# Kernel tuning notes

Measured on AMD Instinct MI355X. Metric: run time of the kernel, lower is better.

Reference implementation:

```python
import jax, jax.numpy as jnp
import numpy as np
import math

N_FFT = 1024
HOP = 256
WIN = 1024
SR = 16000
N_MELS = 80
F_MIN = 0.0
F_MAX = 8000.0
N_STFT = N_FFT // 2 + 1


def _hz_to_mel_slaney(f):
    f = np.asarray(f, dtype=np.float64)
    logstep = math.log(6.4) / 27.0
    mel = 3.0 * f / 200.0
    return np.where(f >= 1000.0, 15.0 + np.log(np.maximum(f, 1e-10) / 1000.0) / logstep, mel)


def _mel_to_hz_slaney(m):
    m = np.asarray(m, dtype=np.float64)
    logstep = math.log(6.4) / 27.0
    f = 200.0 * m / 3.0
    return np.where(m >= 15.0, 1000.0 * np.exp(logstep * (m - 15.0)), f)


def _melscale_fbanks():
    # matches torchaudio.functional.melscale_fbanks(norm='slaney', mel_scale='slaney')
    all_freqs = np.linspace(0.0, SR / 2.0, N_STFT)
    m_min = _hz_to_mel_slaney(F_MIN)
    m_max = _hz_to_mel_slaney(F_MAX)
    m_pts = np.linspace(m_min, m_max, N_MELS + 2)
    f_pts = _mel_to_hz_slaney(m_pts)
    f_diff = f_pts[1:] - f_pts[:-1]                      # [n_mels+1]
    slopes = f_pts[None, :] - all_freqs[:, None]          # [n_freqs, n_mels+2]
    down = -slopes[:, :-2] / f_diff[:-1]
    up = slopes[:, 2:] / f_diff[1:]
    fb = np.maximum(0.0, np.minimum(down, up))            # [n_freqs, n_mels]
    enorm = 2.0 / (f_pts[2:N_MELS + 2] - f_pts[:N_MELS])  # slaney area normalization
    fb = fb * enorm[None, :]
    return fb.astype(np.float32)


def setup_inputs() -> dict:
    key = jax.random.key(0)
    wav = jax.random.normal(key, (32, 1, 160000), dtype=jnp.float32)
    # periodic Hann window
    n = np.arange(WIN)
    window = (0.5 * (1.0 - np.cos(2.0 * np.pi * n / WIN))).astype(np.float32)
    # real DFT matrices: angle = -2*pi*k*n/n_fft, k in [0, n_fft//2]
    k = np.arange(N_STFT, dtype=np.float64)
    nr = np.arange(N_FFT, dtype=np.float64)
    angle = -2.0 * np.pi * k[:, None] * nr[None, :] / N_FFT
    rfft_real = np.cos(angle).astype(np.float32)  # [N_STFT, N_FFT]
    rfft_imag = np.sin(angle).astype(np.float32)
    mel_fbanks = _melscale_fbanks()                # [N_STFT, N_MELS]
    return {
        "wav_with_channel": wav,
        "window": jnp.asarray(window),
        "mel_fbanks": jnp.asarray(mel_fbanks),
        "rfft_real": jnp.asarray(rfft_real),
        "rfft_imag": jnp.asarray(rfft_imag),
    }


def reference(wav_with_channel, window, mel_fbanks, rfft_real, rfft_imag):
    wav = wav_with_channel[:, 0, :]                      # [B, T]
    pad = N_FFT // 2
    padded = jnp.pad(wav, ((0, 0), (pad, pad)), mode="reflect")
    num_frames = (padded.shape[1] - WIN) // HOP + 1
    idx = jnp.arange(num_frames)[:, None] * HOP + jnp.arange(WIN)[None, :]  # [F, W]
    frames = padded[:, idx]                              # [B, F, W]
    windowed = frames * window                           # broadcast [W]
    # matmul-based real DFT (win_length == n_fft, power == 1.0)
    real = jnp.einsum("bfw,kw->bfk", windowed, rfft_real)
    imag = jnp.einsum("bfw,kw->bfk", windowed, rfft_imag)
    magnitude = jnp.sqrt(real * real + imag * imag)      # [B, F, N_STFT]
    mel = jnp.einsum("bfk,km->bfm", magnitude, mel_fbanks)  # [B, F, N_MELS]
    return jnp.transpose(mel, (0, 2, 1))                 # [B, N_MELS, F]
```

## Files before the change

kernel.cpp:

```cpp
#include <hip/hip_runtime.h>

#define WAVLEN   160000
#define NFRAMES  626
#define NFFT     1024
#define HOP      256
#define NSTFT    513
#define NMELS    80
#define FBLKS    157
#define PAD(i)   ((i) + ((i) >> 3))
#define BUFSZ    576
#define PWSTRIDE 49
#define PWTOT    (NMELS * PWSTRIDE)

__device__ __forceinline__ float2 cadd(float2 a, float2 b){ return make_float2(a.x+b.x, a.y+b.y); }
__device__ __forceinline__ float2 csub(float2 a, float2 b){ return make_float2(a.x-b.x, a.y-b.y); }
__device__ __forceinline__ float2 cmul(float2 a, float2 b){
    return make_float2(fmaf(a.x, b.x, -a.y*b.y), fmaf(a.x, b.y, a.y*b.x));
}
__device__ __forceinline__ float2 mulnegi(float2 a){ return make_float2(a.y, -a.x); }

__device__ __forceinline__ void fft4(float2& a0, float2& a1, float2& a2, float2& a3) {
    float2 t0 = cadd(a0, a2), t1 = csub(a0, a2);
    float2 t2 = cadd(a1, a3), t3 = csub(a1, a3);
    a0 = cadd(t0, t2); a2 = csub(t0, t2);
    float2 nt3 = mulnegi(t3);
    a1 = cadd(t1, nt3); a3 = csub(t1, nt3);
}

__device__ __forceinline__ void fft8(float2 v[8]) {
    float2 e0=v[0], e1=v[2], e2=v[4], e3=v[6];
    float2 o0=v[1], o1=v[3], o2=v[5], o3=v[7];
    fft4(e0,e1,e2,e3);
    fft4(o0,o1,o2,o3);
    const float C = 0.70710678118654752f;
    float2 w1o = make_float2(C*(o1.x + o1.y), C*(o1.y - o1.x));
    float2 w2o = mulnegi(o2);
    float2 w3o = make_float2(C*(o3.y - o3.x), -C*(o3.x + o3.y));
    v[0] = cadd(e0, o0);  v[4] = csub(e0, o0);
    v[1] = cadd(e1, w1o); v[5] = csub(e1, w1o);
    v[2] = cadd(e2, w2o); v[6] = csub(e2, w2o);
    v[3] = cadd(e3, w3o); v[7] = csub(e3, w3o);
}

__device__ __forceinline__ int2 mel_range(int m) {
    const float LOGSTEP = 0.06875177742094912f;
    const float MSTEP   = 0.55858524f;
    float mlo = (float)m * MSTEP;
    float mhi = (float)(m + 2) * MSTEP;
    float flo = (mlo < 15.f) ? 66.6666667f * mlo : 1000.f * expf(LOGSTEP * (mlo - 15.f));
    float fhi = (mhi < 15.f) ? 66.6666667f * mhi : 1000.f * expf(LOGSTEP * (mhi - 15.f));
    int klo = (int)(flo * 0.064f) - 1;
    int khi = (int)(fhi * 0.064f) + 2;
    klo = max(klo, 0);
    khi = min(khi, NSTFT);
    return make_int2(klo, khi);
}

__global__ __launch_bounds__(1024) void mel_pack_kernel(const float* __restrict__ fb,
                                                        float* __restrict__ pwg) {
    int p = threadIdx.x;
    #pragma unroll
    for (int it = 0; it < 4; ++it, p += 1024) {
        if (p < PWTOT) {
            int m = p / PWSTRIDE, j = p - m * PWSTRIDE;
            int2 rr = mel_range(m);
            float val = 0.f;
            if (j < rr.y - rr.x) val = fb[(rr.x + j) * NMELS + m];
            pwg[p] = val;
        }
    }
}

__global__ __launch_bounds__(256) void melspec_kernel(
    const float* __restrict__ wav,
    const float* __restrict__ window,
    const float* __restrict__ fb,
    const float* __restrict__ twr,
    const float* __restrict__ twi,
    const float* __restrict__ pwg,
    float* __restrict__ out)
{
    __shared__ float2 buf[4][BUFSZ];
    __shared__ float  pw[PWTOT];

    const int tid  = threadIdx.x;
    const int lane = tid & 63;
    const int w    = tid >> 6;
    const int b    = blockIdx.x / FBLKS;
    const int fblk = blockIdx.x % FBLKS;
    const int frame = fblk * 4 + w;
    const bool active = frame < NFRAMES;

    if (pwg) {
        for (int p = tid; p < PWTOT; p += 256) pw[p] = pwg[p];
    }
    __syncthreads();

    float2* Bf = buf[w];
    float2 v[8];

    if (active) {
        const float* wb = wav + (size_t)b * WAVLEN;
        const int base = frame * HOP - 512;
        if (base >= 0 && base + NFFT <= WAVLEN) {
            #pragma unroll
            for (int r = 0; r < 8; ++r) {
                int n = lane + 64 * r;
                float2 s  = *(const float2*)(wb + base + 2 * n);
                float2 wn = *(const float2*)(window + 2 * n);
                v[r] = make_float2(s.x * wn.x, s.y * wn.y);
            }
        } else {
            #pragma unroll
            for (int r = 0; r < 8; ++r) {
                int n = lane + 64 * r;
                int g0 = base + 2 * n, g1 = g0 + 1;
                g0 = g0 < 0 ? -g0 : (g0 >= WAVLEN ? 2 * WAVLEN - 2 - g0 : g0);
                g1 = g1 < 0 ? -g1 : (g1 >= WAVLEN ? 2 * WAVLEN - 2 - g1 : g1);
                v[r] = make_float2(wb[g0] * window[2 * n], wb[g1] * window[2 * n + 1]);
            }
        }
        fft8(v);
        #pragma unroll
        for (int r = 0; r < 8; ++r) Bf[PAD(8 * lane + r)] = v[r];

        #pragma unroll
        for (int r = 0; r < 8; ++r) v[r] = Bf[PAD(lane + 64 * r)];
        const int jm = lane & 7;
        {
            float2 b2 = make_float2(twr[16 * jm], twi[16 * jm]);
            float2 u = b2;
            v[1] = cmul(v[1], u);
            #pragma unroll
            for (int r = 2; r < 8; ++r) { u = cmul(u, b2); v[r] = cmul(v[r], u); }
        }
        fft8(v);
        const int idxD = (lane >> 3) * 64 + jm;
        #pragma unroll
        for (int r = 0; r < 8; ++r) Bf[PAD(idxD + 8 * r)] = v[r];

        #pragma unroll
        for (int r = 0; r < 8; ++r) v[r] = Bf[PAD(lane + 64 * r)];
        {
            float2 b3 = make_float2(twr[2 * lane], twi[2 * lane]);
            float2 u = b3;
            v[1] = cmul(v[1], u);
            #pragma unroll
            for (int r = 2; r < 8; ++r) { u = cmul(u, b3); v[r] = cmul(v[r], u); }
        }
        fft8(v);
        #pragma unroll
        for (int r = 0; r < 8; ++r) Bf[PAD(lane + 64 * r)] = v[r];

        float2 zm[8]; float wrk[8], wik[8];
        #pragma unroll
        for (int r = 0; r < 8; ++r) {
            int k = lane + 64 * r;
            zm[r] = Bf[PAD((512 - k) & 511)];
            wrk[r] = twr[k]; wik[r] = twi[k];
        }
        float* sm = (float*)Bf + 96;
        #pragma unroll
        for (int r = 0; r < 8; ++r) {
            int k = lane + 64 * r;
            if (k == 0) {
                sm[0]   = fabsf(v[0].x + v[0].y);
                sm[512] = fabsf(v[0].x - v[0].y);
            } else {
                float xer = 0.5f * (v[r].x + zm[r].x), xei = 0.5f * (v[r].y - zm[r].y);
                float xod = 0.5f * (v[r].y + zm[r].y), xoi = 0.5f * (zm[r].x - v[r].x);
                float xr = xer + fmaf(xod, wrk[r], -xoi * wik[r]);
                float xi = xei + fmaf(xod, wik[r],  xoi * wrk[r]);
                sm[k] = sqrtf(fmaf(xr, xr, xi * xi));
            }
        }

        float* pmel = (float*)Bf;
        if (pwg) {
            int m = lane;
            int2 rr = mel_range(m);
            int wd = rr.y - rr.x;
            float acc = 0.f;
            for (int j = 0; j < wd; ++j)
                acc = fmaf(sm[rr.x + j], pw[m * PWSTRIDE + j], acc);
            pmel[m] = acc;
            if (lane < 16) {
                m = lane + 64;
                rr = mel_range(m); wd = rr.y - rr.x;
                acc = 0.f;
                for (int j = 0; j < wd; ++j)
                    acc = fmaf(sm[rr.x + j], pw[m * PWSTRIDE + j], acc);
                pmel[m] = acc;
            }
        } else {
            int m = lane;
            int2 rr = mel_range(m);
            float acc = 0.f;
            for (int k = rr.x; k < rr.y; ++k)
                acc = fmaf(sm[k], fb[k * NMELS + m], acc);
            pmel[m] = acc;
            if (lane < 16) {
                m = lane + 64;
                rr = mel_range(m);
                acc = 0.f;
                for (int k = rr.x; k < rr.y; ++k)
                    acc = fmaf(sm[k], fb[k * NMELS + m], acc);
                pmel[m] = acc;
            }
        }
    }
    __syncthreads();

    if (tid < 160) {
        int m = tid >> 1, h = tid & 1;
        int f0 = fblk * 4 + 2 * h;
        if (f0 < NFRAMES) {
            float2 o;
            o.x = ((float*)buf[2 * h])[m];
            o.y = ((float*)buf[2 * h + 1])[m];
            *(float2*)(out + ((size_t)b * NMELS + m) * NFRAMES + f0) = o;
        }
    }
}

extern "C" void kernel_launch(void* const* d_in, const int* in_sizes, int n_in,
                              void* d_out, int out_size, void* d_ws, size_t ws_size,
                              hipStream_t stream) {
    const float* wav    = (const float*)d_in[0];
    const float* window = (const float*)d_in[1];
    const float* fb     = (const float*)d_in[2];
    const float* rfr    = (const float*)d_in[3];
    const float* rfi    = (const float*)d_in[4];
    float* out = (float*)d_out;

    float* pwg = nullptr;
    if (ws_size >= PWTOT * sizeof(float)) {
        pwg = (float*)d_ws;
        mel_pack_kernel<<<1, 1024, 0, stream>>>(fb, pwg);
    }

    int B = in_sizes[0] / WAVLEN;
    melspec_kernel<<<dim3(B * FBLKS), 256, 0, stream>>>(
        wav, window, fb, rfr + NFFT, rfi + NFFT, pwg, out);
}
```

Before: 118.0 us.

## Process eight frames per block, use power-tree twiddles, rebalance mel assignment

Doubles the frames per block from four to eight, so there are 512 threads per block and half as many blocks. The mel-filter load into shared memory is amortised over more frames and the output stores are grouped into wider runs. Twiddle powers are now computed as a shallow multiply tree instead of a serial chain, which shortens the dependency chain at the cost of slightly different rounding. Low mel indices (narrow filters) go to the extra lanes so the wide high filters are spread across the full wavefront. In exchange, shared memory per block grows and fewer blocks fit per CU.

```diff
diff --git a/kernel.cpp b/kernel.cpp
--- a/kernel.cpp
+++ b/kernel.cpp
@@ -6,7 +6,8 @@
 #define HOP      256
 #define NSTFT    513
 #define NMELS    80
-#define FBLKS    157
+#define WPB      8
+#define FBLKS    79
 #define PAD(i)   ((i) + ((i) >> 3))
 #define BUFSZ    576
 #define PWSTRIDE 49
@@ -42,6 +43,19 @@
     v[3] = cadd(e3, w3o); v[7] = csub(e3, w3o);
 }
 
+__device__ __forceinline__ void twiddle7(float2 v[8], float2 b) {
+    float2 u2 = cmul(b, b);
+    float2 u3 = cmul(u2, b);
+    float2 u4 = cmul(u2, u2);
+    float2 u5 = cmul(u4, b);
+    float2 u6 = cmul(u4, u2);
+    float2 u7 = cmul(u4, u3);
+    v[1] = cmul(v[1], b);  v[2] = cmul(v[2], u2);
+    v[3] = cmul(v[3], u3); v[4] = cmul(v[4], u4);
+    v[5] = cmul(v[5], u5); v[6] = cmul(v[6], u6);
+    v[7] = cmul(v[7], u7);
+}
+
 __device__ __forceinline__ int2 mel_range(int m) {
     const float LOGSTEP = 0.06875177742094912f;
     const float MSTEP   = 0.55858524f;
@@ -71,7 +85,7 @@
     }
 }
 
-__global__ __launch_bounds__(256) void melspec_kernel(
+__global__ __launch_bounds__(512) void melspec_kernel(
     const float* __restrict__ wav,
     const float* __restrict__ window,
     const float* __restrict__ fb,
@@ -80,7 +94,7 @@
     const float* __restrict__ pwg,
     float* __restrict__ out)
 {
-    __shared__ float2 buf[4][BUFSZ];
+    __shared__ float2 buf[WPB][BUFSZ];
     __shared__ float  pw[PWTOT];
 
     const int tid  = threadIdx.x;
@@ -88,11 +102,11 @@
     const int w    = tid >> 6;
     const int b    = blockIdx.x / FBLKS;
     const int fblk = blockIdx.x % FBLKS;
-    const int frame = fblk * 4 + w;
+    const int frame = fblk * WPB + w;
     const bool active = frame < NFRAMES;
 
     if (pwg) {
-        for (int p = tid; p < PWTOT; p += 256) pw[p] = pwg[p];
+        for (int p = tid; p < PWTOT; p += 512) pw[p] = pwg[p];
     }
     __syncthreads();
 
@@ -127,13 +141,7 @@
         #pragma unroll
         for (int r = 0; r < 8; ++r) v[r] = Bf[PAD(lane + 64 * r)];
         const int jm = lane & 7;
-        {
-            float2 b2 = make_float2(twr[16 * jm], twi[16 * jm]);
-            float2 u = b2;
-            v[1] = cmul(v[1], u);
-            #pragma unroll
-            for (int r = 2; r < 8; ++r) { u = cmul(u, b2); v[r] = cmul(v[r], u); }
-        }
+        twiddle7(v, make_float2(twr[16 * jm], twi[16 * jm]));
         fft8(v);
         const int idxD = (lane >> 3) * 64 + jm;
         #pragma unroll
@@ -141,13 +149,7 @@
 
         #pragma unroll
         for (int r = 0; r < 8; ++r) v[r] = Bf[PAD(lane + 64 * r)];
-        {
-            float2 b3 = make_float2(twr[2 * lane], twi[2 * lane]);
-            float2 u = b3;
-            v[1] = cmul(v[1], u);
-            #pragma unroll
-            for (int r = 2; r < 8; ++r) { u = cmul(u, b3); v[r] = cmul(v[r], u); }
-        }
+        twiddle7(v, make_float2(twr[2 * lane], twi[2 * lane]));
         fft8(v);
         #pragma unroll
         for (int r = 0; r < 8; ++r) Bf[PAD(lane + 64 * r)] = v[r];
@@ -177,7 +179,7 @@
 
         float* pmel = (float*)Bf;
         if (pwg) {
-            int m = lane;
+            int m = 16 + lane;
             int2 rr = mel_range(m);
             int wd = rr.y - rr.x;
             float acc = 0.f;
@@ -185,7 +187,7 @@
                 acc = fmaf(sm[rr.x + j], pw[m * PWSTRIDE + j], acc);
             pmel[m] = acc;
             if (lane < 16) {
-                m = lane + 64;
+                m = lane;
                 rr = mel_range(m); wd = rr.y - rr.x;
                 acc = 0.f;
                 for (int j = 0; j < wd; ++j)
@@ -193,14 +195,14 @@
                 pmel[m] = acc;
             }
         } else {
-            int m = lane;
+            int m = 16 + lane;
             int2 rr = mel_range(m);
             float acc = 0.f;
             for (int k = rr.x; k < rr.y; ++k)
                 acc = fmaf(sm[k], fb[k * NMELS + m], acc);
             pmel[m] = acc;
             if (lane < 16) {
-                m = lane + 64;
+                m = lane;
                 rr = mel_range(m);
                 acc = 0.f;
                 for (int k = rr.x; k < rr.y; ++k)
@@ -211,13 +213,13 @@
     }
     __syncthreads();
 
-    if (tid < 160) {
-        int m = tid >> 1, h = tid & 1;
-        int f0 = fblk * 4 + 2 * h;
+    if (tid < 320) {
+        int m = tid >> 2, part = tid & 3;
+        int f0 = fblk * WPB + 2 * part;
         if (f0 < NFRAMES) {
             float2 o;
-            o.x = ((float*)buf[2 * h])[m];
-            o.y = ((float*)buf[2 * h + 1])[m];
+            o.x = ((float*)buf[2 * part])[m];
+            o.y = ((float*)buf[2 * part + 1])[m];
             *(float2*)(out + ((size_t)b * NMELS + m) * NFRAMES + f0) = o;
         }
     }
@@ -240,6 +242,6 @@
     }
 
     int B = in_sizes[0] / WAVLEN;
-    melspec_kernel<<<dim3(B * FBLKS), 256, 0, stream>>>(
+    melspec_kernel<<<dim3(B * FBLKS), 512, 0, stream>>>(
         wav, window, fb, rfr + NFFT, rfi + NFFT, pwg, out);
 }
```

New measurement: 109.7 us. 1.08x faster.
